# Kernel tuning notes

Hardware: AMD Instinct MI355X
Metric: run time of the kernel (lower is better)

The kernel has to match this reference:

```python
import jax, jax.numpy as jnp
import numpy as np

H, D, DK, DV = 16, 1024, 64, 64
B, SQ, SK = 4, 1024, 1024
SCALE = float(np.power(D, 0.5))  # original scales by sqrt(num_dim), not sqrt(num_dim_k)


def setup_inputs() -> dict:
    key = jax.random.key(0)
    ks = jax.random.split(key, 8)
    xav_k = float(np.sqrt(2.0 / (D + DK)))
    xav_v = float(np.sqrt(2.0 / (D + DV)))
    return {
        "query": jax.random.normal(ks[0], (B, SQ, D), jnp.float32),
        "key": jax.random.normal(ks[1], (B, SK, D), jnp.float32),
        "value": jax.random.normal(ks[2], (B, SK, D), jnp.float32),
        "w_q": jax.random.normal(ks[3], (H, D, DK), jnp.float32) * xav_k,
        "w_k": jax.random.normal(ks[4], (H, D, DK), jnp.float32) * xav_k,
        "w_v": jax.random.normal(ks[5], (H, D, DV), jnp.float32) * xav_v,
        "w_proj": jax.random.normal(ks[6], (D, H * DV), jnp.float32) * float(np.sqrt(1.0 / (H * DV))),
        "b_proj": jnp.zeros((D,), jnp.float32),
    }


def reference(query, key, value, w_q, w_k, w_v, w_proj, b_proj):
    # per-head projections: [b,s,d] x [h,d,k] -> [b,h,s,k]
    q = jnp.einsum("bsd,hdk->bhsk", query, w_q)
    k = jnp.einsum("bsd,hdk->bhsk", key, w_k)
    v = jnp.einsum("bsd,hdv->bhsv", value, w_v)
    # scaled dot-product attention (dropout = identity in eval)
    scores = jnp.einsum("bhqk,bhsk->bhqs", q, k) / SCALE
    attn = jax.nn.softmax(scores, axis=-1)  # [b,h,sq,sk]
    out = jnp.einsum("bhqs,bhsv->bhqv", attn, v)
    # original: outs laid out [h*b, sq, dv], split by batch and cat on feature dim
    # -> heads concatenated along last dim: [b, sq, h*dv]
    out = out.transpose(0, 2, 1, 3).reshape(B, SQ, H * DV)
    out = out @ w_proj.T + b_proj  # Linear(H*DV -> D)
    # attns returned with head-major batch: [h*b, sq, sk]
    attns = attn.transpose(1, 0, 2, 3).reshape(H * B, SQ, SK)
    return (out, attns)
```

## Files before the change

kernel.cpp:

```cpp
#include <hip/hip_runtime.h>
#include <cstdint>

typedef __bf16 bf16;
typedef bf16 bf16x8 __attribute__((ext_vector_type(8)));
typedef bf16 bf16x4 __attribute__((ext_vector_type(4)));
typedef float f32x4 __attribute__((ext_vector_type(4)));

#define MFMA16(a, b, c) __builtin_amdgcn_mfma_f32_16x16x32_bf16((a), (b), (c), 0, 0, 0)

#define GLOBAL_TO_LDS16(gptr, lptr)                                          \
  __builtin_amdgcn_global_load_lds(                                          \
      (const __attribute__((address_space(1))) void*)(gptr),                 \
      (__attribute__((address_space(3))) void*)(lptr), 16, 0, 0)


__global__ __launch_bounds__(256) void cvt_all(
    const float* __restrict__ q, const float* __restrict__ k,
    const float* __restrict__ v, const float* __restrict__ wp,
    bf16* __restrict__ qb, bf16* __restrict__ kb,
    bf16* __restrict__ vb, bf16* __restrict__ wpb) {
  long i4 = ((long)blockIdx.x * 256 + threadIdx.x) * 4;
  const float* src;
  bf16* dst;
  long off;
  if (i4 < 4194304) {
    src = q; dst = qb; off = i4;
  } else if (i4 < 8388608) {
    src = k; dst = kb; off = i4 - 4194304;
  } else if (i4 < 12582912) {
    src = v; dst = vb; off = i4 - 8388608;
  } else {
    src = wp; dst = wpb; off = i4 - 12582912;
  }
  float4 f = *(const float4*)(src + off);
  bf16x4 o;
  o[0] = (bf16)f.x; o[1] = (bf16)f.y; o[2] = (bf16)f.z; o[3] = (bf16)f.w;
  *(bf16x4*)(dst + off) = o;
}

__global__ __launch_bounds__(256) void wtrans(
    const float* __restrict__ wq, const float* __restrict__ wk,
    const float* __restrict__ wv, bf16* __restrict__ wqT,
    bf16* __restrict__ wkT, bf16* __restrict__ wvT) {
  __shared__ bf16 tile[64][72];
  int dt = blockIdx.x, h = blockIdx.y, z = blockIdx.z;
  const float* src =
      ((z == 0) ? wq : (z == 1) ? wk : wv) + (long)h * 65536 + dt * 64 * 64;
  bf16* dstM = (z == 0) ? wqT : (z == 1) ? wkT : wvT;
  int t = threadIdx.x;
#pragma unroll
  for (int i = 0; i < 4; ++i) {
    int chunk = t + i * 256;
    int r = chunk >> 4, c4 = chunk & 15;
    float4 f = *(const float4*)(src + r * 64 + c4 * 4);
    bf16x4 o;
    o[0] = (bf16)f.x; o[1] = (bf16)f.y; o[2] = (bf16)f.z; o[3] = (bf16)f.w;
    *(bf16x4*)&tile[r][c4 * 4] = o;
  }
  __syncthreads();
  int kk = t & 63, sc = t >> 6;
  bf16 tmp[16];
#pragma unroll
  for (int j = 0; j < 16; ++j) tmp[j] = tile[sc * 16 + j][kk];
  bf16* dst = dstM + ((long)h * 64 + kk) * 1024 + dt * 64 + sc * 16;
  *(bf16x8*)dst = *(bf16x8*)tmp;
  *(bf16x8*)(dst + 8) = *(bf16x8*)(tmp + 8);
}

__global__ __launch_bounds__(256) void vtrans(const bf16* __restrict__ Vd,
                                              bf16* __restrict__ Vt) {
  __shared__ bf16 tile[64][72];
  int st = blockIdx.x, bh = blockIdx.y;
  const bf16* src = Vd + ((long)bh * 1024 + st * 64) * 64;
  int t = threadIdx.x;
#pragma unroll
  for (int i = 0; i < 2; ++i) {
    int chunk = t + i * 256;
    int r = chunk >> 3, c8 = chunk & 7;
    *(bf16x8*)&tile[r][c8 * 8] = *(const bf16x8*)(src + r * 64 + c8 * 8);
  }
  __syncthreads();
  int d = t & 63, sc = t >> 6;
  bf16 tmp[16];
#pragma unroll
  for (int j = 0; j < 16; ++j) tmp[j] = tile[sc * 16 + j][d];
  bf16* dst = Vt + ((long)bh * 64 + d) * 1024 + st * 64 + sc * 16;
  *(bf16x8*)dst = *(bf16x8*)tmp;
  *(bf16x8*)(dst + 8) = *(bf16x8*)(tmp + 8);
}

__device__ __forceinline__ void gemm_mainloop(
    const bf16* __restrict__ A, const bf16* __restrict__ BT, bf16* As,
    bf16* Bs, int m0, int n0, f32x4 acc[4][4]) {
  const int tid = threadIdx.x;
  const int lane = tid & 63, wave = tid >> 6;
  const int wm = wave >> 1, wn = wave & 1;
  const int ln = lane & 15, ko8 = (lane >> 4) * 8;
  const int c0 = tid, c1 = 256 + tid;
  const int r0 = c0 >> 2, q0 = c0 & 3;
  const int r1 = c1 >> 2, q1 = c1 & 3;

  for (int k0 = 0; k0 < 1024; k0 += 32) {
    GLOBAL_TO_LDS16(A + (long)(m0 + r0) * 1024 + k0 + q0 * 8, As + c0 * 8);
    GLOBAL_TO_LDS16(A + (long)(m0 + r1) * 1024 + k0 + q1 * 8, As + c1 * 8);
    GLOBAL_TO_LDS16(BT + (long)(n0 + r0) * 1024 + k0 + q0 * 8, Bs + c0 * 8);
    GLOBAL_TO_LDS16(BT + (long)(n0 + r1) * 1024 + k0 + q1 * 8, Bs + c1 * 8);
    __syncthreads();
    bf16x8 af[4], bg[4];
#pragma unroll
    for (int t = 0; t < 4; ++t) {
      af[t] = *(const bf16x8*)(As + (wm * 64 + t * 16 + ln) * 32 + ko8);
      bg[t] = *(const bf16x8*)(Bs + (wn * 64 + t * 16 + ln) * 32 + ko8);
    }
#pragma unroll
    for (int i = 0; i < 4; ++i)
#pragma unroll
      for (int j = 0; j < 4; ++j) acc[i][j] = MFMA16(af[i], bg[j], acc[i][j]);
    __syncthreads();
  }
}

__global__ __launch_bounds__(256) void qkv_gemm(
    const bf16* __restrict__ qb, const bf16* __restrict__ kb,
    const bf16* __restrict__ vb, const bf16* __restrict__ wqT,
    const bf16* __restrict__ wkT, const bf16* __restrict__ wvT,
    bf16* __restrict__ Qd, bf16* __restrict__ Kd, bf16* __restrict__ Vd) {
  __shared__ bf16 As[128 * 32];
  __shared__ bf16 Bs[128 * 32];
  int z = blockIdx.z;
  const bf16* A = (z == 0) ? qb : ((z == 1) ? kb : vb);
  const bf16* BT = (z == 0) ? wqT : ((z == 1) ? wkT : wvT);
  int m0 = blockIdx.x * 128, n0 = blockIdx.y * 128;
  f32x4 acc[4][4] = {};
  gemm_mainloop(A, BT, As, Bs, m0, n0, acc);

  const int tid = threadIdx.x, lane = tid & 63, wave = tid >> 6;
  const int wm = wave >> 1, wn = wave & 1, ln = lane & 15, lk = lane >> 4;
  const float alpha = (z == 0) ? 0.03125f : 1.0f;
  bf16* dst = (z == 0) ? Qd : ((z == 1) ? Kd : Vd);
#pragma unroll
  for (int ti = 0; ti < 4; ++ti)
#pragma unroll
    for (int tj = 0; tj < 4; ++tj) {
      int n = n0 + wn * 64 + tj * 16 + ln;
#pragma unroll
      for (int i = 0; i < 4; ++i) {
        int m = m0 + wm * 64 + ti * 16 + lk * 4 + i;
        long addr =
            ((((long)(m >> 10) * 16 + (n >> 6)) << 10) + (m & 1023)) * 64 +
            (n & 63);
        dst[addr] = (bf16)(acc[ti][tj][i] * alpha);
      }
    }
}

__global__ __launch_bounds__(256, 4) void attn_kernel(
    const bf16* __restrict__ Qd, const bf16* __restrict__ Kd,
    const bf16* __restrict__ Vtd, float* __restrict__ attns,
    bf16* __restrict__ Ob) {
  __shared__ bf16 P[16 * 1024];
  __shared__ float wstats[4][16][2];

  int qt = blockIdx.x, h = blockIdx.y, b = blockIdx.z;
  int q0 = qt * 16;
  int tid = threadIdx.x, lane = tid & 63, wave = tid >> 6;
  int ln = lane & 15, lk = lane >> 4;

  const bf16* Qbh = Qd + (((long)(b * 16 + h)) << 10) * 64;
  const bf16* Kbh = Kd + (((long)(b * 16 + h)) << 10) * 64;
  const bf16* Vbh = Vtd + (((long)(b * 16 + h)) << 6) * 1024;

  bf16x8 bq0 = *(const bf16x8*)(Qbh + (long)(q0 + ln) * 64 + lk * 8);
  bf16x8 bq1 = *(const bf16x8*)(Qbh + (long)(q0 + ln) * 64 + 32 + lk * 8);

  f32x4 sacc[16];
  __builtin_amdgcn_s_setprio(1);
#pragma unroll
  for (int t = 0; t < 16; ++t) {
    int sk0 = wave * 256 + t * 16;
    f32x4 a = {0.f, 0.f, 0.f, 0.f};
    bf16x8 ak0 = *(const bf16x8*)(Kbh + (long)(sk0 + ln) * 64 + lk * 8);
    bf16x8 ak1 = *(const bf16x8*)(Kbh + (long)(sk0 + ln) * 64 + 32 + lk * 8);
    a = MFMA16(ak0, bq0, a);
    a = MFMA16(ak1, bq1, a);
    sacc[t] = a;
  }
  __builtin_amdgcn_s_setprio(0);

  float m = sacc[0][0];
#pragma unroll
  for (int t = 0; t < 16; ++t)
#pragma unroll
    for (int i = 0; i < 4; ++i) m = fmaxf(m, sacc[t][i]);
  m = fmaxf(m, __shfl_xor(m, 16, 64));
  m = fmaxf(m, __shfl_xor(m, 32, 64));
  float s = 0.f;
#pragma unroll
  for (int t = 0; t < 16; ++t)
#pragma unroll
    for (int i = 0; i < 4; ++i) {
      float e = __expf(sacc[t][i] - m);
      sacc[t][i] = e;
      s += e;
    }
  s += __shfl_xor(s, 16, 64);
  s += __shfl_xor(s, 32, 64);
  if (lk == 0) {
    wstats[wave][ln][0] = m;
    wstats[wave][ln][1] = s;
  }
  __syncthreads();

  float M = fmaxf(fmaxf(wstats[0][ln][0], wstats[1][ln][0]),
                  fmaxf(wstats[2][ln][0], wstats[3][ln][0]));
  float L = 0.f;
#pragma unroll
  for (int w = 0; w < 4; ++w)
    L += wstats[w][ln][1] * __expf(wstats[w][ln][0] - M);
  float fscale = __expf(m - M) / L;

  float* arow = attns + ((((long)(h * 4 + b)) << 10) + q0 + ln) * 1024 +
                wave * 256 + lk * 4;
#pragma unroll
  for (int t = 0; t < 16; ++t) {
    f32x4 av;
    bf16x4 pv;
#pragma unroll
    for (int i = 0; i < 4; ++i) {
      av[i] = sacc[t][i] * fscale;
      pv[i] = (bf16)av[i];
    }
    *(f32x4*)(arow + t * 16) = av;
    int col = wave * 256 + t * 16 + lk * 4;
    int g = col >> 3;
    *(bf16x4*)(P + (ln << 10) + ((g ^ (ln & 7)) << 3) + (col & 7)) = pv;
  }
  __syncthreads();

  f32x4 oacc = {0.f, 0.f, 0.f, 0.f};
  __builtin_amdgcn_s_setprio(1);
#pragma unroll 4
  for (int s0 = 0; s0 < 1024; s0 += 32) {
    int g = (s0 >> 3) + lk;
    bf16x8 ap = *(const bf16x8*)(P + (ln << 10) + ((g ^ (ln & 7)) << 3));
    bf16x8 bv =
        *(const bf16x8*)(Vbh + (long)(wave * 16 + ln) * 1024 + s0 + lk * 8);
    oacc = MFMA16(ap, bv, oacc);
  }
  __builtin_amdgcn_s_setprio(0);
#pragma unroll
  for (int i = 0; i < 4; ++i) {
    int qrow = q0 + lk * 4 + i;
    Ob[((((long)b) << 10) + qrow) * 1024 + (h << 6) + wave * 16 + ln] =
        (bf16)oacc[i];
  }
}

__global__ __launch_bounds__(256) void out_gemm(
    const bf16* __restrict__ Ob, const bf16* __restrict__ wpb,
    const float* __restrict__ bias, float* __restrict__ out) {
  __shared__ bf16 As[128 * 32];
  __shared__ bf16 Bs[128 * 32];
  int m0 = blockIdx.x * 128, n0 = blockIdx.y * 128;
  f32x4 acc[4][4] = {};
  gemm_mainloop(Ob, wpb, As, Bs, m0, n0, acc);

  const int tid = threadIdx.x, lane = tid & 63, wave = tid >> 6;
  const int wm = wave >> 1, wn = wave & 1, ln = lane & 15, lk = lane >> 4;
#pragma unroll
  for (int ti = 0; ti < 4; ++ti)
#pragma unroll
    for (int tj = 0; tj < 4; ++tj) {
      int n = n0 + wn * 64 + tj * 16 + ln;
      float bn = bias[n];
#pragma unroll
      for (int i = 0; i < 4; ++i) {
        int m = m0 + wm * 64 + ti * 16 + lk * 4 + i;
        out[(long)m * 1024 + n] = acc[ti][tj][i] + bn;
      }
    }
}

extern "C" void kernel_launch(void* const* d_in, const int* in_sizes, int n_in,
                              void* d_out, int out_size, void* d_ws,
                              size_t ws_size, hipStream_t stream) {
  const float* query = (const float*)d_in[0];
  const float* key = (const float*)d_in[1];
  const float* value = (const float*)d_in[2];
  const float* w_q = (const float*)d_in[3];
  const float* w_k = (const float*)d_in[4];
  const float* w_v = (const float*)d_in[5];
  const float* w_proj = (const float*)d_in[6];
  const float* b_proj = (const float*)d_in[7];

  char* ws = (char*)d_ws;
  bf16* qb = (bf16*)(ws);
  bf16* kb = (bf16*)(ws + (8ul << 20));
  bf16* vb = (bf16*)(ws + (16ul << 20));
  bf16* wqT = (bf16*)(ws + (24ul << 20));
  bf16* wkT = (bf16*)(ws + (26ul << 20));
  bf16* wvT = (bf16*)(ws + (28ul << 20));
  bf16* wpb = (bf16*)(ws + (30ul << 20));
  bf16* Qd = (bf16*)(ws + (32ul << 20));
  bf16* Kd = (bf16*)(ws + (40ul << 20));
  bf16* Vtd = (bf16*)(ws + (48ul << 20));
  bf16* Ob = (bf16*)(ws + (56ul << 20));
  bf16* Vd = (bf16*)(ws + (64ul << 20));

  float* out = (float*)d_out;
  float* attns = out + 4194304;

  cvt_all<<<13312, 256, 0, stream>>>(query, key, value, w_proj, qb, kb, vb,
                                     wpb);
  wtrans<<<dim3(16, 16, 3), 256, 0, stream>>>(w_q, w_k, w_v, wqT, wkT, wvT);
  qkv_gemm<<<dim3(32, 8, 3), 256, 0, stream>>>(qb, kb, vb, wqT, wkT, wvT, Qd,
                                               Kd, Vd);
  vtrans<<<dim3(16, 64), 256, 0, stream>>>(Vd, Vtd);
  attn_kernel<<<dim3(64, 16, 4), 256, 0, stream>>>(Qd, Kd, Vtd, attns, Ob);
  out_gemm<<<dim3(32, 8), 256, 0, stream>>>(Ob, wpb, b_proj, out);
}
```

Before: 513.0 us.

## Merge convert and weight-transpose kernels, split PV accumulator, relax attn launch bounds

Folds the fp32-to-bf16 conversion kernel and the weight transpose kernel into a single launch, dispatching by block index, which removes one kernel launch and its gap. The PV loop in the attention kernel now alternates between two independent accumulators to break the MFMA dependency chain. The attention kernel's launch-bounds occupancy hint drops from 4 to 2, giving the compiler more registers but possibly fewer resident waves. Every prep block now reserves the transpose tile in shared memory, even the conversion blocks that never use it.

```diff
diff --git a/kernel.cpp b/kernel.cpp
--- a/kernel.cpp
+++ b/kernel.cpp
@@ -14,40 +14,41 @@
       (__attribute__((address_space(3))) void*)(lptr), 16, 0, 0)
 
 
-__global__ __launch_bounds__(256) void cvt_all(
+__global__ __launch_bounds__(256) void prep(
     const float* __restrict__ q, const float* __restrict__ k,
     const float* __restrict__ v, const float* __restrict__ wp,
-    bf16* __restrict__ qb, bf16* __restrict__ kb,
-    bf16* __restrict__ vb, bf16* __restrict__ wpb) {
-  long i4 = ((long)blockIdx.x * 256 + threadIdx.x) * 4;
-  const float* src;
-  bf16* dst;
-  long off;
-  if (i4 < 4194304) {
-    src = q; dst = qb; off = i4;
-  } else if (i4 < 8388608) {
-    src = k; dst = kb; off = i4 - 4194304;
-  } else if (i4 < 12582912) {
-    src = v; dst = vb; off = i4 - 8388608;
-  } else {
-    src = wp; dst = wpb; off = i4 - 12582912;
-  }
-  float4 f = *(const float4*)(src + off);
-  bf16x4 o;
-  o[0] = (bf16)f.x; o[1] = (bf16)f.y; o[2] = (bf16)f.z; o[3] = (bf16)f.w;
-  *(bf16x4*)(dst + off) = o;
-}
-
-__global__ __launch_bounds__(256) void wtrans(
-    const float* __restrict__ wq, const float* __restrict__ wk,
-    const float* __restrict__ wv, bf16* __restrict__ wqT,
-    bf16* __restrict__ wkT, bf16* __restrict__ wvT) {
+    bf16* __restrict__ qb, bf16* __restrict__ kb, bf16* __restrict__ vb,
+    bf16* __restrict__ wpb, const float* __restrict__ wq,
+    const float* __restrict__ wk, const float* __restrict__ wv,
+    bf16* __restrict__ wqT, bf16* __restrict__ wkT, bf16* __restrict__ wvT) {
   __shared__ bf16 tile[64][72];
-  int dt = blockIdx.x, h = blockIdx.y, z = blockIdx.z;
+  int bx = blockIdx.x;
+  int t = threadIdx.x;
+  if (bx < 13312) {
+    long i4 = ((long)bx * 256 + t) * 4;
+    const float* src;
+    bf16* dst;
+    long off;
+    if (i4 < 4194304) {
+      src = q; dst = qb; off = i4;
+    } else if (i4 < 8388608) {
+      src = k; dst = kb; off = i4 - 4194304;
+    } else if (i4 < 12582912) {
+      src = v; dst = vb; off = i4 - 8388608;
+    } else {
+      src = wp; dst = wpb; off = i4 - 12582912;
+    }
+    float4 f = *(const float4*)(src + off);
+    bf16x4 o;
+    o[0] = (bf16)f.x; o[1] = (bf16)f.y; o[2] = (bf16)f.z; o[3] = (bf16)f.w;
+    *(bf16x4*)(dst + off) = o;
+    return;
+  }
+  int idx = bx - 13312;
+  int dt = idx & 15, h = (idx >> 4) & 15, z = idx >> 8;
   const float* src =
       ((z == 0) ? wq : (z == 1) ? wk : wv) + (long)h * 65536 + dt * 64 * 64;
   bf16* dstM = (z == 0) ? wqT : (z == 1) ? wkT : wvT;
-  int t = threadIdx.x;
 #pragma unroll
   for (int i = 0; i < 4; ++i) {
     int chunk = t + i * 256;
@@ -154,7 +155,7 @@
     }
 }
 
-__global__ __launch_bounds__(256, 4) void attn_kernel(
+__global__ __launch_bounds__(256, 2) void attn_kernel(
     const bf16* __restrict__ Qd, const bf16* __restrict__ Kd,
     const bf16* __restrict__ Vtd, float* __restrict__ attns,
     bf16* __restrict__ Ob) {
@@ -237,17 +238,29 @@
   }
   __syncthreads();
 
-  f32x4 oacc = {0.f, 0.f, 0.f, 0.f};
+  f32x4 oaccA = {0.f, 0.f, 0.f, 0.f};
+  f32x4 oaccB = {0.f, 0.f, 0.f, 0.f};
   __builtin_amdgcn_s_setprio(1);
-#pragma unroll 4
-  for (int s0 = 0; s0 < 1024; s0 += 32) {
-    int g = (s0 >> 3) + lk;
-    bf16x8 ap = *(const bf16x8*)(P + (ln << 10) + ((g ^ (ln & 7)) << 3));
-    bf16x8 bv =
-        *(const bf16x8*)(Vbh + (long)(wave * 16 + ln) * 1024 + s0 + lk * 8);
-    oacc = MFMA16(ap, bv, oacc);
+#pragma unroll 2
+  for (int s0 = 0; s0 < 1024; s0 += 64) {
+    {
+      int g = (s0 >> 3) + lk;
+      bf16x8 ap = *(const bf16x8*)(P + (ln << 10) + ((g ^ (ln & 7)) << 3));
+      bf16x8 bv =
+          *(const bf16x8*)(Vbh + (long)(wave * 16 + ln) * 1024 + s0 + lk * 8);
+      oaccA = MFMA16(ap, bv, oaccA);
+    }
+    {
+      int s1 = s0 + 32;
+      int g = (s1 >> 3) + lk;
+      bf16x8 ap = *(const bf16x8*)(P + (ln << 10) + ((g ^ (ln & 7)) << 3));
+      bf16x8 bv =
+          *(const bf16x8*)(Vbh + (long)(wave * 16 + ln) * 1024 + s1 + lk * 8);
+      oaccB = MFMA16(ap, bv, oaccB);
+    }
   }
   __builtin_amdgcn_s_setprio(0);
+  f32x4 oacc = oaccA + oaccB;
 #pragma unroll
   for (int i = 0; i < 4; ++i) {
     int qrow = q0 + lk * 4 + i;
@@ -310,9 +323,8 @@
   float* out = (float*)d_out;
   float* attns = out + 4194304;
 
-  cvt_all<<<13312, 256, 0, stream>>>(query, key, value, w_proj, qb, kb, vb,
-                                     wpb);
-  wtrans<<<dim3(16, 16, 3), 256, 0, stream>>>(w_q, w_k, w_v, wqT, wkT, wvT);
+  prep<<<14080, 256, 0, stream>>>(query, key, value, w_proj, qb, kb, vb, wpb,
+                                  w_q, w_k, w_v, wqT, wkT, wvT);
   qkv_gemm<<<dim3(32, 8, 3), 256, 0, stream>>>(qb, kb, vb, wqT, wkT, wvT, Qd,
                                                Kd, Vd);
   vtrans<<<dim3(16, 64), 256, 0, stream>>>(Vd, Vtd);
```

Result: no change. 513.5 us (+0.1%).
